# Performance work log

Hardware: AMD Instinct MI355X
Metric: run time of the kernel (lower is better)

The kernel has to match this reference:

```python
import jax, jax.numpy as jnp
import numpy as np

NEG = -1e9
SLOPE = 0.2  # LeakyReLU slope (GAT convention)


def setup_inputs() -> dict:
    key = jax.random.key(0)
    ks = jax.random.split(key, 10)
    T, N, E, F, Hd = 32, 512, 64, 64, 64
    x = jax.random.normal(ks[0], (T, N, F), dtype=jnp.float32)
    # Hyperedge incidence [N, E]; guarantee every node is in >= 1 hyperedge.
    Hm = (jax.random.uniform(ks[1], (N, E)) < (2.0 / E)).astype(jnp.int32)
    Hm = Hm.at[jnp.arange(N), jnp.arange(N) % E].set(1)
    # Industry adjacency [N, N] with self loops.
    adj = (jax.random.uniform(ks[2], (N, N)) < 0.05).astype(jnp.int32)
    adj = adj.at[jnp.arange(N), jnp.arange(N)].set(1)
    sc = 0.1
    W = jax.random.normal(ks[3], (F, Hd), jnp.float32) * sc
    a_hyp = jax.random.normal(ks[4], (Hd,), jnp.float32) * sc
    a_ind = jax.random.normal(ks[5], (Hd,), jnp.float32) * sc
    Wc1 = jax.random.normal(ks[6], (Hd, Hd), jnp.float32) * sc
    bc1 = jnp.zeros((Hd,), jnp.float32)
    wc2 = jax.random.normal(ks[7], (Hd,), jnp.float32) * sc
    bc2 = jnp.zeros((), jnp.float32)
    return dict(x=x, H=Hm, adj=adj, nhid=Hd, W=W, a_hyp=a_hyp, a_ind=a_ind,
                Wc1=Wc1, bc1=bc1, wc2=wc2, bc2=bc2)


def _edgeconv(feats, mask, Wc1, bc1, wc2, bc2):
    """Attention pooling over the second-to-last (set) axis.
    feats: [..., K, Hd], mask: broadcastable to [..., K] (bool). -> [..., Hd]"""
    z = jnp.maximum(feats @ Wc1 + bc1, 0.0) @ wc2 + bc2  # [..., K]
    z = jnp.where(mask, z, NEG)
    alpha = jax.nn.softmax(z, axis=-1)
    return jnp.einsum('...k,...kd->...d', alpha, feats)


def reference(x, H, adj, nhid, W, a_hyp, a_ind, Wc1, bc1, wc2, bc2):
    # x: [T, N, F]; H: [N, E] incidence; adj: [N, N]. Eval mode: dropout = id.
    Hb = H.astype(bool)          # [N, E]
    Ab = adj.astype(bool)        # [N, N]
    h = x @ W                    # [T, N, Hd]

    # --- hyperedge_attn: intra-hyperedge node attention (GAT-style) ---
    s_hyp = jax.nn.leaky_relu(h @ a_hyp, SLOPE)                 # [T, N]
    logits = jnp.where(Hb[None, :, :], s_hyp[:, :, None], NEG)  # [T, N, E]
    alpha = jax.nn.softmax(logits, axis=1)                      # over nodes in edge
    # per-(edge,node) contribution; original layout [E,T,N,Hd] -> here [T,N,E,Hd]
    all_hyper = jax.nn.elu(alpha[..., None] * h[:, :, None, :])  # [T, N, E, Hd]

    # --- industry attention over adj ---
    s_ind = jax.nn.leaky_relu(h @ a_ind, SLOPE)                   # [T, N]
    li = jnp.where(Ab[None, :, :], s_ind[:, None, :], NEG)        # [T, N, N]
    beta = jax.nn.softmax(li, axis=-1)
    industry = jnp.einsum('tij,tjd->tid', beta, h)                # [T, N, Hd]

    # --- per-node loop, vectorized ---
    # y8: EdgeConv over the hyperedges containing each node (mask = H row).
    # When a node has exactly 1 hyperedge, masked softmax selects it exactly,
    # which reproduces the original else-branch.
    y8 = _edgeconv(all_hyper, Hb[None, :, :], Wc1, bc1, wc2, bc2)  # [T, N, Hd]
    pair = jnp.stack([industry, y8], axis=2)                       # [T, N, 2, Hd]
    y9 = _edgeconv(pair, jnp.ones((1, 1, 2), bool), Wc1, bc1, wc2, bc2)
    return y9                                                      # [T, N, Hd]
```

## Files before the change

kernel.cpp:

```cpp
#include <hip/hip_runtime.h>

#define T_DIM 32
#define N_DIM 512
#define E_DIM 64
#define F_DIM 64
#define HD    64
#define NBR_CAP 128

static_assert(E_DIM == 64 && HD == 64 && F_DIM == 64, "wave-mapped dims");

__device__ __forceinline__ float wave_sum(float v) {
    #pragma unroll
    for (int off = 32; off > 0; off >>= 1) v += __shfl_xor(v, off, 64);
    return v;
}
__device__ __forceinline__ void wave_sum2(float& a, float& b) {
    #pragma unroll
    for (int off = 32; off > 0; off >>= 1) {
        a += __shfl_xor(a, off, 64);
        b += __shfl_xor(b, off, 64);
    }
}

#define K1_R 16
#define K1_ROWBLK (T_DIM * N_DIM / K1_R)
#define K1_CSRBLK (N_DIM / 4)
__global__ __launch_bounds__(256) void k1_h_s(
    const float* __restrict__ x, const float* __restrict__ W,
    const float* __restrict__ a_hyp, const float* __restrict__ a_ind,
    const int* __restrict__ adj,
    float* __restrict__ h, float* __restrict__ s_hyp, float* __restrict__ s_ind,
    int* __restrict__ degs, int* __restrict__ nbrs)
{
    const int wave = threadIdx.x >> 6;
    const int lane = threadIdx.x & 63;

    if (blockIdx.x < K1_ROWBLK) {
        __shared__ float xl[K1_R * F_DIM];
        const int row0 = blockIdx.x * K1_R;
        ((float4*)xl)[threadIdx.x] =
            ((const float4*)(x + (size_t)row0 * F_DIM))[threadIdx.x];
        float wcol[F_DIM];
        #pragma unroll
        for (int f = 0; f < F_DIM; ++f) wcol[f] = W[f * HD + lane];
        const float ah = a_hyp[lane], ai = a_ind[lane];
        __syncthreads();
        #pragma unroll
        for (int r = wave; r < K1_R; r += 4) {
            float a0 = 0.f, a1 = 0.f, a2 = 0.f, a3 = 0.f;
            #pragma unroll
            for (int f = 0; f < F_DIM; f += 4) {
                const float4 xv = *(const float4*)&xl[r * F_DIM + f];
                a0 = fmaf(xv.x, wcol[f + 0], a0);
                a1 = fmaf(xv.y, wcol[f + 1], a1);
                a2 = fmaf(xv.z, wcol[f + 2], a2);
                a3 = fmaf(xv.w, wcol[f + 3], a3);
            }
            const float acc = (a0 + a1) + (a2 + a3);
            h[(size_t)(row0 + r) * HD + lane] = acc;
            float sh = acc * ah, si = acc * ai;
            wave_sum2(sh, si);
            if (lane == 0) {
                s_hyp[row0 + r] = sh > 0.f ? sh : 0.2f * sh;
                s_ind[row0 + r] = si > 0.f ? si : 0.2f * si;
            }
        }
    } else {
        const int i = (blockIdx.x - K1_ROWBLK) * 4 + wave;
        int deg = 0;
        #pragma unroll
        for (int c = 0; c < N_DIM / 64; ++c) {
            const int j = c * 64 + lane;
            const bool bit = adj[(size_t)i * N_DIM + j] != 0;
            const unsigned long long mask = __ballot(bit);
            if (bit) {
                const int pos = deg + __popcll(mask & ((1ull << lane) - 1ull));
                nbrs[i * NBR_CAP + pos] = j;
            }
            deg += __popcll(mask);
        }
        if (lane == 0) degs[i] = deg;
    }
}

__global__ __launch_bounds__(256) void k23_stats_industry(
    const int* __restrict__ Hm, const int* __restrict__ degs,
    const int* __restrict__ nbrs,
    const float* __restrict__ s_hyp, const float* __restrict__ s_ind,
    const float* __restrict__ h,
    float* __restrict__ d_e, float* __restrict__ industry)
{
    const int wave = threadIdx.x >> 6;
    const int lane = threadIdx.x & 63;

    if (blockIdx.x < T_DIM) {
        const int t = blockIdx.x;
        __shared__ float exps[N_DIM];
        __shared__ float departial[4][E_DIM];
        #pragma unroll
        for (int c = 0; c < N_DIM / 256; ++c)
            exps[c * 256 + threadIdx.x] = expf(s_hyp[t * N_DIM + c * 256 + threadIdx.x]);
        __syncthreads();
        float de = 0.f;
        const int n0 = wave * (N_DIM / 4);
        #pragma unroll 4
        for (int k = 0; k < N_DIM / 4; ++k) {
            const int n = n0 + k;
            const int m = Hm[n * E_DIM + lane];
            de += m ? exps[n] : 0.f;
        }
        departial[wave][lane] = de;
        __syncthreads();
        if (wave == 0)
            d_e[t * E_DIM + lane] = (departial[0][lane] + departial[1][lane])
                                  + (departial[2][lane] + departial[3][lane]);
    } else {
        __shared__ int   jl[4][64];
        __shared__ float el[4][64];
        const int idx = (blockIdx.x - T_DIM) * 4 + wave;
        const int t = idx >> 9, i = idx & (N_DIM - 1);
        const int deg = degs[i];
        const int* nb = nbrs + i * NBR_CAP;
        const float* st = s_ind + t * N_DIM;
        const float* hbase = h + (size_t)t * N_DIM * HD;
        float evp = 0.f, ac0 = 0.f, ac1 = 0.f, ac2 = 0.f, ac3 = 0.f;
        for (int base = 0; base < deg; base += 64) {
            const int k = base + lane;
            const bool valid = k < deg;
            const int j = valid ? nb[k] : 0;
            const float ev = valid ? expf(st[j]) : 0.f;
            evp += ev;
            jl[wave][lane] = j;
            el[wave][lane] = ev;
            const int cnt = min(deg - base, 64);
            const int cnt8 = (cnt + 7) & ~7;
            for (int kk = 0; kk < cnt8; kk += 8) {
                const int   j0 = jl[wave][kk + 0], j1 = jl[wave][kk + 1];
                const int   j2 = jl[wave][kk + 2], j3 = jl[wave][kk + 3];
                const int   j4 = jl[wave][kk + 4], j5 = jl[wave][kk + 5];
                const int   j6 = jl[wave][kk + 6], j7 = jl[wave][kk + 7];
                const float w0 = el[wave][kk + 0], w1 = el[wave][kk + 1];
                const float w2 = el[wave][kk + 2], w3 = el[wave][kk + 3];
                const float w4 = el[wave][kk + 4], w5 = el[wave][kk + 5];
                const float w6 = el[wave][kk + 6], w7 = el[wave][kk + 7];
                const float v0 = hbase[(size_t)j0 * HD + lane];
                const float v1 = hbase[(size_t)j1 * HD + lane];
                const float v2 = hbase[(size_t)j2 * HD + lane];
                const float v3 = hbase[(size_t)j3 * HD + lane];
                const float v4 = hbase[(size_t)j4 * HD + lane];
                const float v5 = hbase[(size_t)j5 * HD + lane];
                const float v6 = hbase[(size_t)j6 * HD + lane];
                const float v7 = hbase[(size_t)j7 * HD + lane];
                ac0 = fmaf(w0, v0, ac0);
                ac1 = fmaf(w1, v1, ac1);
                ac2 = fmaf(w2, v2, ac2);
                ac3 = fmaf(w3, v3, ac3);
                ac0 = fmaf(w4, v4, ac0);
                ac1 = fmaf(w5, v5, ac1);
                ac2 = fmaf(w6, v6, ac2);
                ac3 = fmaf(w7, v7, ac3);
            }
        }
        const float evsum = wave_sum(evp);
        industry[(size_t)idx * HD + lane] = ((ac0 + ac1) + (ac2 + ac3)) / evsum;
    }
}

__global__ __launch_bounds__(256) void k4_final(
    const int* __restrict__ Hm, const float* __restrict__ s_hyp,
    const float* __restrict__ d_e,
    const float* __restrict__ h, const float* __restrict__ industry,
    const float* __restrict__ Wc1, const float* __restrict__ bc1,
    const float* __restrict__ wc2, const float* __restrict__ bc2,
    float* __restrict__ out)
{
    __shared__ float fl[4 * 2 * HD];
    const int wave = threadIdx.x >> 6;
    const int lane = threadIdx.x & 63;
    const int idx  = blockIdx.x * 4 + wave;
    const int t = idx >> 9, n = idx & (N_DIM - 1);
    float* fw = fl + wave * 2 * HD;

    float wreg[HD];
    #pragma unroll
    for (int d = 0; d < HD; ++d) wreg[d] = Wc1[d * HD + lane];
    const float bc1v = bc1[lane];
    const float wc2v = wc2[lane];
    const float bc2v = bc2[0];

    const float hv = h[(size_t)idx * HD + lane];
    const float esh = expf(s_hyp[idx]);

    const int memv = Hm[n * E_DIM + lane];
    const float alpha = memv ? esh * __frcp_rn(d_e[t * E_DIM + lane]) : 0.f;
    unsigned long long mk = __ballot(memv != 0);

    float zsum = 0.f, acc = 0.f;
    while (mk) {
        const int e0 = __ffsll((long long)mk) - 1; mk &= mk - 1;
        const bool have1 = mk != 0;
        const int e1 = have1 ? __ffsll((long long)mk) - 1 : e0;
        if (have1) mk &= mk - 1;
        const float a0 = __shfl(alpha, e0, 64);
        const float a1 = __shfl(alpha, e1, 64);
        float f0 = a0 * hv; f0 = f0 > 0.f ? f0 : expm1f(f0);
        float f1 = a1 * hv; f1 = f1 > 0.f ? f1 : expm1f(f1);
        fw[lane]      = f0;
        fw[HD + lane] = f1;
        float u0 = 0.f, u1 = 0.f, u2 = 0.f, u3 = 0.f;
        float v0 = 0.f, v1 = 0.f, v2 = 0.f, v3 = 0.f;
        #pragma unroll
        for (int d = 0; d < HD; d += 4) {
            const float4 A = *(const float4*)&fw[d];
            const float4 B = *(const float4*)&fw[HD + d];
            u0 = fmaf(A.x, wreg[d + 0], u0);
            u1 = fmaf(A.y, wreg[d + 1], u1);
            u2 = fmaf(A.z, wreg[d + 2], u2);
            u3 = fmaf(A.w, wreg[d + 3], u3);
            v0 = fmaf(B.x, wreg[d + 0], v0);
            v1 = fmaf(B.y, wreg[d + 1], v1);
            v2 = fmaf(B.z, wreg[d + 2], v2);
            v3 = fmaf(B.w, wreg[d + 3], v3);
        }
        float p = fmaxf((u0 + u1) + (u2 + u3) + bc1v, 0.f) * wc2v;
        float q = fmaxf((v0 + v1) + (v2 + v3) + bc1v, 0.f) * wc2v;
        wave_sum2(p, q);
        const float w0 = expf(p + bc2v);
        const float w1 = have1 ? expf(q + bc2v) : 0.f;
        zsum += w0 + w1;
        acc = fmaf(w0, f0, acc);
        acc = fmaf(w1, f1, acc);
    }
    const float y8 = acc / zsum;

    const float indv = industry[(size_t)idx * HD + lane];
    fw[lane]      = indv;
    fw[HD + lane] = y8;
    float p0 = 0.f, p1 = 0.f, q0 = 0.f, q1 = 0.f;
    #pragma unroll
    for (int d = 0; d < HD; d += 4) {
        const float4 iv = *(const float4*)&fw[d];
        const float4 yv = *(const float4*)&fw[HD + d];
        p0 = fmaf(iv.x, wreg[d + 0], p0);
        p1 = fmaf(iv.y, wreg[d + 1], p1);
        p0 = fmaf(iv.z, wreg[d + 2], p0);
        p1 = fmaf(iv.w, wreg[d + 3], p1);
        q0 = fmaf(yv.x, wreg[d + 0], q0);
        q1 = fmaf(yv.y, wreg[d + 1], q1);
        q0 = fmaf(yv.z, wreg[d + 2], q0);
        q1 = fmaf(yv.w, wreg[d + 3], q1);
    }
    float zp = fmaxf(p0 + p1 + bc1v, 0.f) * wc2v;
    float zq = fmaxf(q0 + q1 + bc1v, 0.f) * wc2v;
    wave_sum2(zp, zq);
    const float w0 = expf(zp + bc2v), w1 = expf(zq + bc2v);
    out[(size_t)idx * HD + lane] = fmaf(w0, indv, w1 * y8) / (w0 + w1);
}

extern "C" void kernel_launch(void* const* d_in, const int* in_sizes, int n_in,
                              void* d_out, int out_size, void* d_ws, size_t ws_size,
                              hipStream_t stream) {
    const float* x     = (const float*)d_in[0];
    const int*   Hm    = (const int*)  d_in[1];
    const int*   adj   = (const int*)  d_in[2];
    const float* W     = (const float*)d_in[4];
    const float* a_hyp = (const float*)d_in[5];
    const float* a_ind = (const float*)d_in[6];
    const float* Wc1   = (const float*)d_in[7];
    const float* bc1   = (const float*)d_in[8];
    const float* wc2   = (const float*)d_in[9];
    const float* bc2   = (const float*)d_in[10];
    float* out = (float*)d_out;

    float* ws       = (float*)d_ws;
    float* h        = ws;
    float* s_hyp    = h + (size_t)T_DIM * N_DIM * HD;
    float* s_ind    = s_hyp + T_DIM * N_DIM;
    float* d_e      = s_ind + T_DIM * N_DIM;
    float* industry = d_e + T_DIM * E_DIM;
    int*   degs     = (int*)(industry + (size_t)T_DIM * N_DIM * HD);
    int*   nbrs     = degs + N_DIM;

    k1_h_s<<<K1_ROWBLK + K1_CSRBLK, 256, 0, stream>>>(
        x, W, a_hyp, a_ind, adj, h, s_hyp, s_ind, degs, nbrs);
    k23_stats_industry<<<T_DIM + T_DIM * N_DIM / 4, 256, 0, stream>>>(
        Hm, degs, nbrs, s_hyp, s_ind, h, d_e, industry);
    k4_final<<<T_DIM * N_DIM / 4, 256, 0, stream>>>(
        Hm, s_hyp, d_e, h, industry, Wc1, bc1, wc2, bc2, out);
}
```

Before: 156.0 us.

## Vectorize industry gather with float4 lane groups and XCD-aware block mapping

Measured after the change: 155.1 us. Within noise of the previous version (-0.6%).

```diff
diff --git a/kernel.cpp b/kernel.cpp
--- a/kernel.cpp
+++ b/kernel.cpp
@@ -117,13 +117,21 @@
     } else {
         __shared__ int   jl[4][64];
         __shared__ float el[4][64];
-        const int idx = (blockIdx.x - T_DIM) * 4 + wave;
-        const int t = idx >> 9, i = idx & (N_DIM - 1);
+        const int B   = blockIdx.x - T_DIM;
+        const int xcd = B & 7;
+        const int pos = B >> 3;
+        const int t   = xcd * 4 + (pos >> 7);
+        const int i   = ((pos & 127) << 2) + wave;
+        const int idx = (t << 9) + i;
+        const int grp = lane >> 4, sub = lane & 15;
+
         const int deg = degs[i];
         const int* nb = nbrs + i * NBR_CAP;
         const float* st = s_ind + t * N_DIM;
         const float* hbase = h + (size_t)t * N_DIM * HD;
-        float evp = 0.f, ac0 = 0.f, ac1 = 0.f, ac2 = 0.f, ac3 = 0.f;
+
+        float evp = 0.f;
+        float4 acc = {0.f, 0.f, 0.f, 0.f};
         for (int base = 0; base < deg; base += 64) {
             const int k = base + lane;
             const bool valid = k < deg;
@@ -133,36 +141,51 @@
             jl[wave][lane] = j;
             el[wave][lane] = ev;
             const int cnt = min(deg - base, 64);
-            const int cnt8 = (cnt + 7) & ~7;
-            for (int kk = 0; kk < cnt8; kk += 8) {
-                const int   j0 = jl[wave][kk + 0], j1 = jl[wave][kk + 1];
-                const int   j2 = jl[wave][kk + 2], j3 = jl[wave][kk + 3];
-                const int   j4 = jl[wave][kk + 4], j5 = jl[wave][kk + 5];
-                const int   j6 = jl[wave][kk + 6], j7 = jl[wave][kk + 7];
-                const float w0 = el[wave][kk + 0], w1 = el[wave][kk + 1];
-                const float w2 = el[wave][kk + 2], w3 = el[wave][kk + 3];
-                const float w4 = el[wave][kk + 4], w5 = el[wave][kk + 5];
-                const float w6 = el[wave][kk + 6], w7 = el[wave][kk + 7];
-                const float v0 = hbase[(size_t)j0 * HD + lane];
-                const float v1 = hbase[(size_t)j1 * HD + lane];
-                const float v2 = hbase[(size_t)j2 * HD + lane];
-                const float v3 = hbase[(size_t)j3 * HD + lane];
-                const float v4 = hbase[(size_t)j4 * HD + lane];
-                const float v5 = hbase[(size_t)j5 * HD + lane];
-                const float v6 = hbase[(size_t)j6 * HD + lane];
-                const float v7 = hbase[(size_t)j7 * HD + lane];
-                ac0 = fmaf(w0, v0, ac0);
-                ac1 = fmaf(w1, v1, ac1);
-                ac2 = fmaf(w2, v2, ac2);
-                ac3 = fmaf(w3, v3, ac3);
-                ac0 = fmaf(w4, v4, ac0);
-                ac1 = fmaf(w5, v5, ac1);
-                ac2 = fmaf(w6, v6, ac2);
-                ac3 = fmaf(w7, v7, ac3);
+            for (int kk = 0; kk < cnt; kk += 16) {
+                const int   j0 = jl[wave][kk + grp];
+                const int   j1 = jl[wave][kk + 4 + grp];
+                const int   j2 = jl[wave][kk + 8 + grp];
+                const int   j3 = jl[wave][kk + 12 + grp];
+                const float w0 = el[wave][kk + grp];
+                const float w1 = el[wave][kk + 4 + grp];
+                const float w2 = el[wave][kk + 8 + grp];
+                const float w3 = el[wave][kk + 12 + grp];
+                const float4 v0 = *(const float4*)&hbase[(size_t)j0 * HD + sub * 4];
+                const float4 v1 = *(const float4*)&hbase[(size_t)j1 * HD + sub * 4];
+                const float4 v2 = *(const float4*)&hbase[(size_t)j2 * HD + sub * 4];
+                const float4 v3 = *(const float4*)&hbase[(size_t)j3 * HD + sub * 4];
+                acc.x = fmaf(w0, v0.x, acc.x);
+                acc.y = fmaf(w0, v0.y, acc.y);
+                acc.z = fmaf(w0, v0.z, acc.z);
+                acc.w = fmaf(w0, v0.w, acc.w);
+                acc.x = fmaf(w1, v1.x, acc.x);
+                acc.y = fmaf(w1, v1.y, acc.y);
+                acc.z = fmaf(w1, v1.z, acc.z);
+                acc.w = fmaf(w1, v1.w, acc.w);
+                acc.x = fmaf(w2, v2.x, acc.x);
+                acc.y = fmaf(w2, v2.y, acc.y);
+                acc.z = fmaf(w2, v2.z, acc.z);
+                acc.w = fmaf(w2, v2.w, acc.w);
+                acc.x = fmaf(w3, v3.x, acc.x);
+                acc.y = fmaf(w3, v3.y, acc.y);
+                acc.z = fmaf(w3, v3.z, acc.z);
+                acc.w = fmaf(w3, v3.w, acc.w);
             }
         }
+        #pragma unroll
+        for (int off = 16; off <= 32; off <<= 1) {
+            acc.x += __shfl_xor(acc.x, off, 64);
+            acc.y += __shfl_xor(acc.y, off, 64);
+            acc.z += __shfl_xor(acc.z, off, 64);
+            acc.w += __shfl_xor(acc.w, off, 64);
+        }
         const float evsum = wave_sum(evp);
-        industry[(size_t)idx * HD + lane] = ((ac0 + ac1) + (ac2 + ac3)) / evsum;
+        if (grp == 0) {
+            const float r = __frcp_rn(evsum);
+            float4 o;
+            o.x = acc.x * r; o.y = acc.y * r; o.z = acc.z * r; o.w = acc.w * r;
+            *(float4*)&industry[(size_t)idx * HD + sub * 4] = o;
+        }
     }
 }
 
```
